# Kernel tuning notes

Hardware: AMD Instinct MI355X
Metric: run time of the kernel (lower is better)

Reference implementation:

```python
import jax, jax.numpy as jnp
import numpy as np

B, N, DIM, H = 64, 196, 1024, 32
HD = DIM // H  # 32, must equal H for the bias broadcast quirk
S = 14  # sqrt(num_patches)


def _relative_position_index(s):
    coords = np.stack(np.meshgrid(np.arange(s), np.arange(s), indexing='ij'))  # [2,s,s]
    cf = coords.reshape(2, -1)  # [2, N]
    rel = (cf[:, :, None] - cf[:, None, :]).transpose(1, 2, 0)  # [N,N,2]
    rel[..., 0] += s - 1
    rel[..., 1] += s - 1
    rel[..., 0] *= 2 * s - 1
    return rel.sum(-1).astype(np.int32)  # [N,N], values in [0, (2s-1)^2)


def setup_inputs() -> dict:
    key = jax.random.key(0)
    k0, k1, k2, k3 = jax.random.split(key, 4)
    x = jax.random.normal(k0, (B, N, DIM), dtype=jnp.float32)
    W_qkv = jax.random.normal(k1, (DIM, 3 * DIM), dtype=jnp.float32) * 0.02
    W_proj = jax.random.normal(k2, (DIM, DIM), dtype=jnp.float32) * 0.02
    b_proj = jnp.zeros((DIM,), dtype=jnp.float32)
    rpk = jax.random.normal(k3, ((2 * S - 1) ** 2, HD), dtype=jnp.float32)  # [729, HD]
    rel_idx = jnp.asarray(_relative_position_index(S))  # [N, N] int32
    return {"x": x, "W_qkv": W_qkv, "W_proj": W_proj, "b_proj": b_proj,
            "rpk": rpk, "rel_idx": rel_idx}


def reference(x, W_qkv, W_proj, b_proj, rpk, rel_idx):
    b, n, c = x.shape
    scale = HD ** -0.5
    qkv = (x @ W_qkv).reshape(b, n, 3, H, HD)  # [B,N,3,H,HD]
    q, k, v = jnp.moveaxis(qkv, 2, 0)          # each [B,N,H,HD]
    q = q.transpose(0, 2, 1, 3)                # [B,H,N,HD]
    k = k.transpose(0, 2, 1, 3)
    v = v.transpose(0, 2, 1, 3)
    attn = jnp.einsum('bhnd,bhmd->bhnm', q, k) * scale  # [B,H,N,N]
    # gather relative-position bias: [N*N, HD] -> [N,N,HD] -> [HD,N,N]
    bias = rpk[rel_idx.reshape(-1)].reshape(n, n, HD).transpose(2, 0, 1)
    attn = jax.nn.softmax(attn + bias[None], axis=-1)   # bias broadcasts since HD == H
    out = jnp.einsum('bhnm,bhmd->bhnd', attn, v)        # [B,H,N,HD]
    out = out.transpose(0, 2, 1, 3).reshape(b, n, c)    # [B,N,C]
    return out @ W_proj + b_proj
```

## Files before the change

### kernel.cpp

```cpp
#include <hip/hip_runtime.h>
#include <hip/hip_bf16.h>

typedef __bf16 bf16_t;
typedef __attribute__((ext_vector_type(8))) __bf16 bf16x8;
typedef __attribute__((ext_vector_type(4))) __bf16 bf16x4;
typedef __attribute__((ext_vector_type(4))) float f32x4;

#define NPOS 38416
#define NPAD 224

__device__ __forceinline__ void async_copy16(const bf16_t* g, bf16_t* l) {
  __builtin_amdgcn_global_load_lds((const __attribute__((address_space(1))) void*)g,
                                   (__attribute__((address_space(3))) void*)l, 16, 0, 0);
}

__global__ __launch_bounds__(256) void cast_x_kernel(const float* __restrict__ x,
                                                     bf16_t* __restrict__ xb, int n4) {
  int i = blockIdx.x * 256 + threadIdx.x;
  if (i < n4) {
    float4 v = ((const float4*)x)[i];
    bf16x4 o;
    o[0] = (bf16_t)v.x; o[1] = (bf16_t)v.y; o[2] = (bf16_t)v.z; o[3] = (bf16_t)v.w;
    ((bf16x4*)xb)[i] = o;
  }
}

__global__ __launch_bounds__(256) void transpose_cast_kernel(const float* __restrict__ src,
                                                             bf16_t* __restrict__ dst,
                                                             int K, int Ncols) {
  __shared__ float tile[32][33];
  int t = threadIdx.x;
  int tx = t & 31, ty = t >> 5;
  int bx = blockIdx.x, by = blockIdx.y;
  for (int r = ty; r < 32; r += 8)
    tile[r][tx] = src[(size_t)(by * 32 + r) * Ncols + bx * 32 + tx];
  __syncthreads();
  for (int r = ty; r < 32; r += 8)
    dst[(size_t)(bx * 32 + r) * K + by * 32 + tx] = (bf16_t)tile[tx][r];
}

__global__ __launch_bounds__(256) void bias_gather_kernel(const float* __restrict__ rpk,
                                                          const int* __restrict__ rel_idx,
                                                          float* __restrict__ bias) {
  int pos = blockIdx.x * 256 + threadIdx.x;
  if (pos < NPOS) {
    int idx = rel_idx[pos];
    const float* r = rpk + idx * 32;
#pragma unroll
    for (int h = 0; h < 32; ++h) bias[h * NPOS + pos] = r[h];
  }
}

template <int MODE>
__global__ __launch_bounds__(256, 2) void gemm_bt_kernel(
    const bf16_t* __restrict__ A, const bf16_t* __restrict__ Bt,
    bf16_t* __restrict__ qo, bf16_t* __restrict__ ko, bf16_t* __restrict__ vto,
    float* __restrict__ fo, const float* __restrict__ bp) {
  constexpr int K = 1024;
  __shared__ alignas(16) bf16_t As[128 * 32];
  __shared__ alignas(16) bf16_t Bs[128 * 32];
  const int t = threadIdx.x;
  const int lane = t & 63;
  const int quad = lane >> 4;
  const int l16 = lane & 15;
  const int wave = t >> 6;
  const int m0 = blockIdx.x * 128, n0 = blockIdx.y * 128;
  const int wr = (wave >> 1) * 64, wc = (wave & 1) * 64;

  const int c0 = t, c1 = t + 256;
  const bf16_t* gA0 = A + (size_t)(m0 + (c0 >> 2)) * K + (c0 & 3) * 8;
  const bf16_t* gA1 = A + (size_t)(m0 + (c1 >> 2)) * K + (c1 & 3) * 8;
  const bf16_t* gB0 = Bt + (size_t)(n0 + (c0 >> 2)) * K + (c0 & 3) * 8;
  const bf16_t* gB1 = Bt + (size_t)(n0 + (c1 >> 2)) * K + (c1 & 3) * 8;
  bf16_t* lA0 = As + c0 * 8;
  bf16_t* lA1 = As + c1 * 8;
  bf16_t* lB0 = Bs + c0 * 8;
  bf16_t* lB1 = Bs + c1 * 8;

  const f32x4 vzero = {0.f, 0.f, 0.f, 0.f};
  f32x4 acc[4][4];
#pragma unroll
  for (int i = 0; i < 4; ++i)
#pragma unroll
    for (int j = 0; j < 4; ++j) acc[i][j] = vzero;

  for (int kt = 0; kt < K; kt += 32) {
    __syncthreads();
    async_copy16(gA0 + kt, lA0);
    async_copy16(gA1 + kt, lA1);
    async_copy16(gB0 + kt, lB0);
    async_copy16(gB1 + kt, lB1);
    __syncthreads();
    bf16x8 af[4], bfr[4];
#pragma unroll
    for (int i = 0; i < 4; ++i) {
      af[i] = *(const bf16x8*)(As + (wr + i * 16 + l16) * 32 + quad * 8);
      bfr[i] = *(const bf16x8*)(Bs + (wc + i * 16 + l16) * 32 + quad * 8);
    }
#pragma unroll
    for (int i = 0; i < 4; ++i)
#pragma unroll
      for (int j = 0; j < 4; ++j)
        acc[i][j] = __builtin_amdgcn_mfma_f32_16x16x32_bf16(af[i], bfr[j], acc[i][j], 0, 0, 0);
  }

  if (MODE == 0) {
    const float qscale = 0.17677669529663687f;
    const int which = n0 >> 10;
#pragma unroll
    for (int i = 0; i < 4; ++i) {
      const int rb = m0 + wr + i * 16 + quad * 4;
#pragma unroll
      for (int j = 0; j < 4; ++j) {
        const int c = n0 + wc + j * 16 + l16;
        const int h = (c >> 5) & 31, d = c & 31;
#pragma unroll
        for (int r = 0; r < 4; ++r) {
          const int rg = rb + r;
          const int b = rg / 196, n = rg - b * 196;
          const float v = acc[i][j][r];
          if (which == 0)
            qo[(((size_t)b * 32 + h) * 196 + n) * 32 + d] = (bf16_t)(v * qscale);
          else if (which == 1)
            ko[(((size_t)b * 32 + h) * 196 + n) * 32 + d] = (bf16_t)v;
          else
            vto[(((size_t)b * 32 + h) * 32 + d) * 196 + n] = (bf16_t)v;
        }
      }
    }
  } else {
#pragma unroll
    for (int i = 0; i < 4; ++i) {
      const int rb = m0 + wr + i * 16 + quad * 4;
#pragma unroll
      for (int j = 0; j < 4; ++j) {
        const int c = n0 + wc + j * 16 + l16;
        const float bias_c = bp[c];
#pragma unroll
        for (int r = 0; r < 4; ++r)
          fo[(size_t)(rb + r) * 1024 + c] = acc[i][j][r] + bias_c;
      }
    }
  }
}

__global__ __launch_bounds__(256, 2) void attn_kernel(
    const bf16_t* __restrict__ q, const bf16_t* __restrict__ kmat,
    const bf16_t* __restrict__ vtg, const float* __restrict__ bias,
    bf16_t* __restrict__ attn_out) {
  __shared__ alignas(16) bf16_t kf[NPAD * 32];
  __shared__ alignas(16) bf16_t vts[32 * NPAD];
  __shared__ alignas(16) bf16_t pb[4][16 * NPAD];

  const int t = threadIdx.x;
  const int lane = t & 63;
  const int quad = lane >> 4, l16 = lane & 15;
  const int wave = t >> 6;
  const int bh = blockIdx.x;
  const int b = bh >> 5, h = bh & 31;
  const bf16_t* qg = q + (size_t)bh * (196 * 32);
  const bf16_t* kg = kmat + (size_t)bh * (196 * 32);
  const bf16_t* vg = vtg + (size_t)bh * (32 * 196);
  const float* bg = bias + (size_t)h * NPOS;

  {
    const uint4* src = (const uint4*)kg;
    uint4* dst = (uint4*)kf;
    for (int c = t; c < 784; c += 256) dst[c] = src[c];
    const uint4 z4 = {0u, 0u, 0u, 0u};
    for (int c = 784 + t; c < 896; c += 256) dst[c] = z4;
    const uint2 z2 = {0u, 0u};
    for (int i = t; i < 1792; i += 256) {
      int d = i / 56, c = i - d * 56;
      uint2 val = (c < 49) ? ((const uint2*)(vg + d * 196))[c] : z2;
      ((uint2*)(vts + d * NPAD))[c] = val;
    }
  }
  __syncthreads();

  const f32x4 vzero = {0.f, 0.f, 0.f, 0.f};
  bf16_t* pw = &pb[wave][0];

  for (int ch = wave; ch < 13; ch += 4) {
    const int q0 = ch * 16;
    int qrow = q0 + l16;
    if (qrow > 195) qrow = 195;
    const bf16x8 aq = *(const bf16x8*)(qg + qrow * 32 + quad * 8);

    f32x4 s[13];
#pragma unroll
    for (int ct = 0; ct < 13; ++ct) {
      const bf16x8 bk = *(const bf16x8*)(kf + (ct * 16 + l16) * 32 + quad * 8);
      s[ct] = __builtin_amdgcn_mfma_f32_16x16x32_bf16(aq, bk, vzero, 0, 0, 0);
    }
#pragma unroll
    for (int ct = 0; ct < 13; ++ct) {
      const int col = ct * 16 + l16;
#pragma unroll
      for (int r = 0; r < 4; ++r) {
        int br = q0 + quad * 4 + r;
        if (br > 195) br = 195;
        if (col < 196)
          s[ct][r] += bg[br * 196 + col];
        else
          s[ct][r] = -1e30f;
      }
    }
    float mx[4], inv[4];
#pragma unroll
    for (int r = 0; r < 4; ++r) {
      float m = s[0][r];
#pragma unroll
      for (int ct = 1; ct < 13; ++ct) m = fmaxf(m, s[ct][r]);
      m = fmaxf(m, __shfl_xor(m, 1));
      m = fmaxf(m, __shfl_xor(m, 2));
      m = fmaxf(m, __shfl_xor(m, 4));
      m = fmaxf(m, __shfl_xor(m, 8));
      mx[r] = m;
    }
#pragma unroll
    for (int ct = 0; ct < 13; ++ct)
#pragma unroll
      for (int r = 0; r < 4; ++r) s[ct][r] = __expf(s[ct][r] - mx[r]);
#pragma unroll
    for (int r = 0; r < 4; ++r) {
      float sum = s[0][r];
#pragma unroll
      for (int ct = 1; ct < 13; ++ct) sum += s[ct][r];
      sum += __shfl_xor(sum, 1);
      sum += __shfl_xor(sum, 2);
      sum += __shfl_xor(sum, 4);
      sum += __shfl_xor(sum, 8);
      inv[r] = 1.f / sum;
    }
#pragma unroll
    for (int ct = 0; ct < 13; ++ct) {
      const int col = ct * 16 + l16;
#pragma unroll
      for (int r = 0; r < 4; ++r) pw[(quad * 4 + r) * NPAD + col] = (bf16_t)s[ct][r];
    }
    if (lane < 32) {
      const bf16x8 z8 = {};
      *(bf16x8*)(pw + (lane >> 1) * NPAD + 208 + (lane & 1) * 8) = z8;
    }
#pragma unroll
    for (int dt = 0; dt < 2; ++dt) {
      f32x4 o = vzero;
#pragma unroll
      for (int kk = 0; kk < 7; ++kk) {
        const bf16x8 ap = *(const bf16x8*)(pw + l16 * NPAD + kk * 32 + quad * 8);
        const bf16x8 bv = *(const bf16x8*)(vts + (dt * 16 + l16) * NPAD + kk * 32 + quad * 8);
        o = __builtin_amdgcn_mfma_f32_16x16x32_bf16(ap, bv, o, 0, 0, 0);
      }
      const int d = dt * 16 + l16;
#pragma unroll
      for (int r = 0; r < 4; ++r) {
        const int n = q0 + quad * 4 + r;
        if (n < 196)
          attn_out[(((size_t)b * 196 + n) * 32 + h) * 32 + d] = (bf16_t)(o[r] * inv[r]);
      }
    }
  }
}

extern "C" void kernel_launch(void* const* d_in, const int* in_sizes, int n_in,
                              void* d_out, int out_size, void* d_ws, size_t ws_size,
                              hipStream_t stream) {
  (void)in_sizes; (void)n_in; (void)out_size; (void)ws_size;
  const float* x = (const float*)d_in[0];
  const float* Wqkv = (const float*)d_in[1];
  const float* Wproj = (const float*)d_in[2];
  const float* bproj = (const float*)d_in[3];
  const float* rpk = (const float*)d_in[4];
  const int* rel_idx = (const int*)d_in[5];
  float* out = (float*)d_out;

  char* ws = (char*)d_ws;
  bf16_t* xb = (bf16_t*)(ws + 0);
  bf16_t* wqkvT = (bf16_t*)(ws + 25690112);
  bf16_t* wprojT = (bf16_t*)(ws + 31981568);
  bf16_t* q = (bf16_t*)(ws + 34078720);
  bf16_t* kk = (bf16_t*)(ws + 59768832);
  bf16_t* vt = (bf16_t*)(ws + 85458944);
  float* bias = (float*)(ws + 111149056);
  bf16_t* attn = xb;

  cast_x_kernel<<<12544, 256, 0, stream>>>(x, xb, 12845056 / 4);
  transpose_cast_kernel<<<dim3(96, 32), 256, 0, stream>>>(Wqkv, wqkvT, 1024, 3072);
  transpose_cast_kernel<<<dim3(32, 32), 256, 0, stream>>>(Wproj, wprojT, 1024, 1024);
  bias_gather_kernel<<<151, 256, 0, stream>>>(rpk, rel_idx, bias);
  gemm_bt_kernel<0><<<dim3(98, 24), 256, 0, stream>>>(xb, wqkvT, q, kk, vt, nullptr, nullptr);
  attn_kernel<<<2048, 256, 0, stream>>>(q, kk, vt, bias, attn);
  gemm_bt_kernel<1><<<dim3(98, 8), 256, 0, stream>>>(attn, wprojT, nullptr, nullptr, nullptr, out, bproj);
}
```

Before: 375.0 us.

## Swizzle GEMM LDS tiles, pad attention LDS strides, reorder grid and prefetch bias

The GEMM now loads each global 16-byte chunk into an XOR-swizzled slot and reads it back with the same swizzle, which is meant to remove LDS bank conflicts in the fragment loads. The GEMM grid is also transposed so blocks that are adjacent in launch order share the same A row tile, which should improve L2 reuse. In the attention kernel, the K, V and P shared buffers get padded row strides (40 and 232) to reduce bank conflicts. The relative-position bias loads are hoisted ahead of the QK MFMAs so their global latency can overlap the matrix math. The changes raise LDS use and register pressure in the attention kernel.

```diff
diff --git a/kernel.cpp b/kernel.cpp
--- a/kernel.cpp
+++ b/kernel.cpp
@@ -8,6 +8,8 @@
 
 #define NPOS 38416
 #define NPAD 224
+#define KSTR 40
+#define VSTR 232
 
 __device__ __forceinline__ void async_copy16(const bf16_t* g, bf16_t* l) {
   __builtin_amdgcn_global_load_lds((const __attribute__((address_space(1))) void*)g,
@@ -64,18 +66,22 @@
   const int quad = lane >> 4;
   const int l16 = lane & 15;
   const int wave = t >> 6;
-  const int m0 = blockIdx.x * 128, n0 = blockIdx.y * 128;
+  const int m0 = blockIdx.y * 128, n0 = blockIdx.x * 128;
   const int wr = (wave >> 1) * 64, wc = (wave & 1) * 64;
 
   const int c0 = t, c1 = t + 256;
-  const bf16_t* gA0 = A + (size_t)(m0 + (c0 >> 2)) * K + (c0 & 3) * 8;
-  const bf16_t* gA1 = A + (size_t)(m0 + (c1 >> 2)) * K + (c1 & 3) * 8;
-  const bf16_t* gB0 = Bt + (size_t)(n0 + (c0 >> 2)) * K + (c0 & 3) * 8;
-  const bf16_t* gB1 = Bt + (size_t)(n0 + (c1 >> 2)) * K + (c1 & 3) * 8;
+  const int sc0 = (c0 & 3) ^ ((c0 >> 3) & 3);
+  const int sc1 = (c1 & 3) ^ ((c1 >> 3) & 3);
+  const bf16_t* gA0 = A + (size_t)(m0 + (c0 >> 2)) * K + sc0 * 8;
+  const bf16_t* gA1 = A + (size_t)(m0 + (c1 >> 2)) * K + sc1 * 8;
+  const bf16_t* gB0 = Bt + (size_t)(n0 + (c0 >> 2)) * K + sc0 * 8;
+  const bf16_t* gB1 = Bt + (size_t)(n0 + (c1 >> 2)) * K + sc1 * 8;
   bf16_t* lA0 = As + c0 * 8;
   bf16_t* lA1 = As + c1 * 8;
   bf16_t* lB0 = Bs + c0 * 8;
   bf16_t* lB1 = Bs + c1 * 8;
+
+  const int qa = quad ^ ((l16 >> 1) & 3);
 
   const f32x4 vzero = {0.f, 0.f, 0.f, 0.f};
   f32x4 acc[4][4];
@@ -94,8 +100,8 @@
     bf16x8 af[4], bfr[4];
 #pragma unroll
     for (int i = 0; i < 4; ++i) {
-      af[i] = *(const bf16x8*)(As + (wr + i * 16 + l16) * 32 + quad * 8);
-      bfr[i] = *(const bf16x8*)(Bs + (wc + i * 16 + l16) * 32 + quad * 8);
+      af[i] = *(const bf16x8*)(As + (wr + i * 16 + l16) * 32 + qa * 8);
+      bfr[i] = *(const bf16x8*)(Bs + (wc + i * 16 + l16) * 32 + qa * 8);
     }
 #pragma unroll
     for (int i = 0; i < 4; ++i)
@@ -148,9 +154,9 @@
     const bf16_t* __restrict__ q, const bf16_t* __restrict__ kmat,
     const bf16_t* __restrict__ vtg, const float* __restrict__ bias,
     bf16_t* __restrict__ attn_out) {
-  __shared__ alignas(16) bf16_t kf[NPAD * 32];
-  __shared__ alignas(16) bf16_t vts[32 * NPAD];
-  __shared__ alignas(16) bf16_t pb[4][16 * NPAD];
+  __shared__ alignas(16) bf16_t kf[NPAD * KSTR];
+  __shared__ alignas(16) bf16_t vts[32 * VSTR];
+  __shared__ alignas(16) bf16_t pb[4][16 * VSTR];
 
   const int t = threadIdx.x;
   const int lane = t & 63;
@@ -166,14 +172,17 @@
   {
     const uint4* src = (const uint4*)kg;
     uint4* dst = (uint4*)kf;
-    for (int c = t; c < 784; c += 256) dst[c] = src[c];
+    for (int c = t; c < 784; c += 256) dst[(c >> 2) * 5 + (c & 3)] = src[c];
     const uint4 z4 = {0u, 0u, 0u, 0u};
-    for (int c = 784 + t; c < 896; c += 256) dst[c] = z4;
+    if (t < 112) {
+      int r = 196 + (t >> 2), ch = t & 3;
+      dst[r * 5 + ch] = z4;
+    }
     const uint2 z2 = {0u, 0u};
     for (int i = t; i < 1792; i += 256) {
       int d = i / 56, c = i - d * 56;
       uint2 val = (c < 49) ? ((const uint2*)(vg + d * 196))[c] : z2;
-      ((uint2*)(vts + d * NPAD))[c] = val;
+      ((uint2*)(vts + d * VSTR))[c] = val;
     }
   }
   __syncthreads();
@@ -187,12 +196,7 @@
     if (qrow > 195) qrow = 195;
     const bf16x8 aq = *(const bf16x8*)(qg + qrow * 32 + quad * 8);
 
-    f32x4 s[13];
-#pragma unroll
-    for (int ct = 0; ct < 13; ++ct) {
-      const bf16x8 bk = *(const bf16x8*)(kf + (ct * 16 + l16) * 32 + quad * 8);
-      s[ct] = __builtin_amdgcn_mfma_f32_16x16x32_bf16(aq, bk, vzero, 0, 0, 0);
-    }
+    float bv[13][4];
 #pragma unroll
     for (int ct = 0; ct < 13; ++ct) {
       const int col = ct * 16 + l16;
@@ -200,8 +204,23 @@
       for (int r = 0; r < 4; ++r) {
         int br = q0 + quad * 4 + r;
         if (br > 195) br = 195;
+        bv[ct][r] = (col < 196) ? bg[br * 196 + col] : 0.f;
+      }
+    }
+
+    f32x4 s[13];
+#pragma unroll
+    for (int ct = 0; ct < 13; ++ct) {
+      const bf16x8 bk = *(const bf16x8*)(kf + (ct * 16 + l16) * KSTR + quad * 8);
+      s[ct] = __builtin_amdgcn_mfma_f32_16x16x32_bf16(aq, bk, vzero, 0, 0, 0);
+    }
+#pragma unroll
+    for (int ct = 0; ct < 13; ++ct) {
+      const int col = ct * 16 + l16;
+#pragma unroll
+      for (int r = 0; r < 4; ++r) {
         if (col < 196)
-          s[ct][r] += bg[br * 196 + col];
+          s[ct][r] += bv[ct][r];
         else
           s[ct][r] = -1e30f;
       }
@@ -237,20 +256,20 @@
     for (int ct = 0; ct < 13; ++ct) {
       const int col = ct * 16 + l16;
 #pragma unroll
-      for (int r = 0; r < 4; ++r) pw[(quad * 4 + r) * NPAD + col] = (bf16_t)s[ct][r];
+      for (int r = 0; r < 4; ++r) pw[(quad * 4 + r) * VSTR + col] = (bf16_t)s[ct][r];
     }
     if (lane < 32) {
       const bf16x8 z8 = {};
-      *(bf16x8*)(pw + (lane >> 1) * NPAD + 208 + (lane & 1) * 8) = z8;
+      *(bf16x8*)(pw + (lane >> 1) * VSTR + 208 + (lane & 1) * 8) = z8;
     }
 #pragma unroll
     for (int dt = 0; dt < 2; ++dt) {
       f32x4 o = vzero;
 #pragma unroll
       for (int kk = 0; kk < 7; ++kk) {
-        const bf16x8 ap = *(const bf16x8*)(pw + l16 * NPAD + kk * 32 + quad * 8);
-        const bf16x8 bv = *(const bf16x8*)(vts + (dt * 16 + l16) * NPAD + kk * 32 + quad * 8);
-        o = __builtin_amdgcn_mfma_f32_16x16x32_bf16(ap, bv, o, 0, 0, 0);
+        const bf16x8 ap = *(const bf16x8*)(pw + l16 * VSTR + kk * 32 + quad * 8);
+        const bf16x8 bv2 = *(const bf16x8*)(vts + (dt * 16 + l16) * VSTR + kk * 32 + quad * 8);
+        o = __builtin_amdgcn_mfma_f32_16x16x32_bf16(ap, bv2, o, 0, 0, 0);
       }
       const int d = dt * 16 + l16;
 #pragma unroll
@@ -289,7 +308,7 @@
   transpose_cast_kernel<<<dim3(96, 32), 256, 0, stream>>>(Wqkv, wqkvT, 1024, 3072);
   transpose_cast_kernel<<<dim3(32, 32), 256, 0, stream>>>(Wproj, wprojT, 1024, 1024);
   bias_gather_kernel<<<151, 256, 0, stream>>>(rpk, rel_idx, bias);
-  gemm_bt_kernel<0><<<dim3(98, 24), 256, 0, stream>>>(xb, wqkvT, q, kk, vt, nullptr, nullptr);
+  gemm_bt_kernel<0><<<dim3(24, 98), 256, 0, stream>>>(xb, wqkvT, q, kk, vt, nullptr, nullptr);
   attn_kernel<<<2048, 256, 0, stream>>>(q, kk, vt, bias, attn);
-  gemm_bt_kernel<1><<<dim3(98, 8), 256, 0, stream>>>(attn, wprojT, nullptr, nullptr, nullptr, out, bproj);
-}
+  gemm_bt_kernel<1><<<dim3(8, 98), 256, 0, stream>>>(attn, wprojT, nullptr, nullptr, nullptr, out, bproj);
+}
```

Result: faster. 356.4 us (-5.0%).
